# Optimization experiments

Hardware: AMD Instinct MI355X
Metric: run time of the kernel (lower is better)

The kernel has to match this reference:

```python
import jax, jax.numpy as jnp
import numpy as np

H = 224          # image height (self.shape[0])
W_IMG = 224      # image width (self.shape[1])
CELLS = 7        # mask_generator num_cells
PAD = CELLS // 2 # reflect pad size
D = 512          # encoder feature dim
NUM_BATCHES = 30
BATCH = 100
EPS = 1e-8       # torch CosineSimilarity eps


def _encode(xb, Wenc):
    # stand-in encoder: 32x32 block average pool -> [B,3,7,7] -> linear to D
    B = xb.shape[0]
    feats = xb.reshape(B, 3, CELLS, H // CELLS, CELLS, W_IMG // CELLS).mean(axis=(3, 5))
    return feats.reshape(B, -1) @ Wenc  # [B, D]


def _cosine(a, b):
    # a: [1,D] (h_star), b: [B,D]; matches nn.CosineSimilarity(dim=1)
    num = jnp.sum(a * b, axis=1)
    den = jnp.maximum(jnp.linalg.norm(a, axis=1) * jnp.linalg.norm(b, axis=1), EPS)
    return num / den  # [B]


def _make_masks(grid, sx, sy):
    # grid: [B,1,7,7] binary floats; bilinear upsample, reflect pad, shifted crop
    B = grid.shape[0]
    up = jax.image.resize(grid, (B, 1, H, W_IMG), method='linear')
    padded = jnp.pad(up, ((0, 0), (0, 0), (PAD, PAD), (PAD, PAD)), mode='reflect')
    crop = jax.vmap(
        lambda g, i, j: jax.lax.dynamic_slice(g, (0, i, j), (1, H, W_IMG))
    )(padded, sx, sy)
    return crop  # [B,1,H,W]


def _relax(x, Wenc, grids, shifts_x, shifts_y):
    h_star = _encode(x, Wenc)  # [1, D]
    R0 = jnp.zeros((H, W_IMG), jnp.float32)
    U0 = jnp.zeros_like(R0)
    sow0 = jnp.full((H, W_IMG), 1e-10, jnp.float32)

    def sample_step(carry, inp):
        # sequential weighted running-mean / Welford variance update
        R, U, sow = carry
        s, m = inp  # s: scalar sim, m: [H,W] mask
        sow = sow + m
        R_new = R + m * (s - R) / sow
        U = U + (s - R_new) * (s - R) * m
        return (R_new, U, sow), None

    def batch_step(carry, binp):
        grid, sx, sy = binp
        masks = _make_masks(grid, sx, sy)        # [B,1,H,W]
        x_mask = x * masks                       # fill_vals_zeros=True path
        h = _encode(x_mask, Wenc)                # [B,D]
        sims = _cosine(h_star, h)                # [B]
        carry, _ = jax.lax.scan(sample_step, carry, (sims, masks[:, 0]))
        return carry, None

    (R, U, sow), _ = jax.lax.scan(batch_step, (R0, U0, sow0),
                                  (grids, shifts_x, shifts_y))
    uncertainty = U / (sow - 1.0)
    return jnp.stack([R, uncertainty])  # [2,H,W]: importance, uncertainty


def setup_inputs() -> dict:
    key = jax.random.key(0)
    k1, k2, k3, k4, k5 = jax.random.split(key, 5)
    x = jax.random.normal(k1, (1, 3, H, W_IMG), jnp.float32)
    Wenc = jax.random.normal(k2, (3 * CELLS * CELLS, D), jnp.float32) * 0.05
    grids = (jax.random.uniform(k3, (NUM_BATCHES, BATCH, 1, CELLS, CELLS)) < 0.5).astype(jnp.float32)
    shifts_x = jax.random.randint(k4, (NUM_BATCHES, BATCH), 0, CELLS)
    shifts_y = jax.random.randint(k5, (NUM_BATCHES, BATCH), 0, CELLS)
    return {"x": x, "Wenc": Wenc, "grids": grids,
            "shifts_x": shifts_x, "shifts_y": shifts_y}


def reference(x, Wenc, grids, shifts_x, shifts_y):
    return _relax(x, Wenc, grids, shifts_x, shifts_y)
```

## Files before the change

kernel.cpp:

```cpp
#include <hip/hip_runtime.h>
#include <math.h>

#define NS 3000
#define NF 147
#define ND 512
#define NSIG 49
#define NSAMP 4
#define NHBLK 750

#define OFF_WT     0
#define OFF_FEATS  6272
#define OFF_V      6432
#define OFF_T      236928
#define OFF_G      589952

__device__ __forceinline__ void wt_compute(int sigma, int p, int& i0c, int& i1c,
                                           float& w0, float& w1) {
  int k = p + sigma - 3;
  int r = k < 0 ? -k : (k > 223 ? 446 - k : k);
  float tc = (float)(2 * r - 31) * (1.0f / 64.0f);
  float fl = floorf(tc);
  int i0 = (int)fl;
  float fr = tc - fl;
  i0c = min(max(i0, 0), 6);
  i1c = min(max(i0 + 1, 0), 6);
  w0 = 1.0f - fr;
  w1 = fr;
}

__global__ void __launch_bounds__(256) k_initV(const float* __restrict__ x,
                                               float* __restrict__ ws) {
  int b = blockIdx.x;
  int t = threadIdx.x;
  if (b < NF) {
    int c = b / 49, rem = b % 49, cy = rem / 7, cx = rem % 7;
    float acc = 0.f;
    for (int idx = t; idx < 1024; idx += 256) {
      int yy = idx >> 5, xx = idx & 31;
      acc += x[(c * 224 + cy * 32 + yy) * 224 + cx * 32 + xx];
    }
    for (int off = 32; off; off >>= 1) acc += __shfl_down(acc, off);
    __shared__ float red[4];
    int wave = t >> 6, lane = t & 63;
    if (lane == 0) red[wave] = acc;
    __syncthreads();
    if (t == 0) ws[OFF_FEATS + b] = (red[0] + red[1] + red[2] + red[3]) * (1.0f / 1024.0f);
  } else if (b == NF) {
    float4* WT = (float4*)(ws + OFF_WT);
    for (int e = t; e < 7 * 224; e += 256) {
      int sigma = e / 224, p = e % 224;
      int i0c, i1c; float w0, w1;
      wt_compute(sigma, p, i0c, i1c, w0, w1);
      WT[e] = make_float4(w0, w1, __int_as_float(i0c), __int_as_float(i1c));
    }
  } else {
    int tid = (b - NF - 1) * 256 + t;
    if (tid >= 7 * 3 * 224 * 7) return;
    int cx = tid % 7;
    int y  = (tid / 7) % 224;
    int c  = (tid / (7 * 224)) % 3;
    int sy = tid / (7 * 224 * 3);
    float acc[7];
    #pragma unroll
    for (int g = 0; g < 7; ++g) acc[g] = 0.f;
    const float* xrow = x + (c * 224 + y) * 224;
    for (int x0 = 0; x0 < 32; ++x0) {
      int px = cx * 32 + x0;
      int i0, i1; float w0, w1;
      wt_compute(sy, px, i0, i1, w0, w1);
      float v = xrow[px];
      #pragma unroll
      for (int g = 0; g < 7; ++g) {
        float w = (g == i0 ? w0 : 0.f) + (g == i1 ? w1 : 0.f);
        acc[g] = fmaf(w, v, acc[g]);
      }
    }
    float* Vp = ws + OFF_V + (((sy * 3 + c) * 224 + y) * 49 + cx * 7);
    #pragma unroll
    for (int g = 0; g < 7; ++g) Vp[g] = acc[g];
  }
}

__global__ void __launch_bounds__(256) k_T(float* __restrict__ ws) {
  int tid = blockIdx.x * blockDim.x + threadIdx.x;
  if (tid >= NSIG * NF * 49) {
    int e = tid - NSIG * NF * 49;
    if (e < 7203) ws[OFF_G + e] = 0.f;
    return;
  }
  int g = tid % 49;
  int f = (tid / 49) % NF;
  int sig = tid / (49 * NF);
  int sx = sig / 7, sy = sig % 7;
  int gy = g / 7, gx = g % 7;
  int c = f / 49, rem = f % 49, cy = rem / 7, cx = rem % 7;
  const float4* WT = (const float4*)(ws + OFF_WT);
  const float* V = ws + OFF_V + ((sy * 3 + c) * 224) * 49 + cx * 7 + gx;
  float acc = 0.f;
  for (int y0 = 0; y0 < 32; ++y0) {
    int y = cy * 32 + y0;
    float4 wt = WT[sx * 224 + y];
    int i0 = __float_as_int(wt.z), i1 = __float_as_int(wt.w);
    float w = (gy == i0 ? wt.x : 0.f) + (gy == i1 ? wt.y : 0.f);
    acc = fmaf(w, V[y * 49], acc);
  }
  ws[OFF_T + (sig * 49 + g) * NF + f] = acc * (1.0f / 1024.0f);
}

__global__ void __launch_bounds__(256) k_H2s(const float* __restrict__ Wenc,
                                             const float* __restrict__ grids,
                                             const int* __restrict__ shx,
                                             const int* __restrict__ shy,
                                             float* __restrict__ ws) {
  __shared__ __align__(16) float sF[NF * NSAMP];
  __shared__ float sGr[NSAMP * 49];
  __shared__ float sFeat[NF];
  __shared__ int   sSig[NSAMP];
  __shared__ float sRed[2][NSAMP][4];
  __shared__ float sRedH[4];
  __shared__ float sS[NSAMP];
  int t = threadIdx.x;
  int b = blockIdx.x;
  int i0s = b * NSAMP;
  for (int e = t; e < NSAMP * 49; e += 256) sGr[e] = grids[i0s * 49 + e];
  if (t < NSAMP) sSig[t] = shx[i0s + t] * 7 + shy[i0s + t];
  if (t < NF) sFeat[t] = ws[OFF_FEATS + t];
  __syncthreads();
  for (int idx = t; idx < NF * NSAMP; idx += 256) {
    int r = idx / NF, f = idx - r * NF;
    const float* T2 = ws + OFF_T + sSig[r] * (49 * NF) + f;
    const float* gr = sGr + r * 49;
    float acc = 0.f;
    #pragma unroll
    for (int g = 0; g < 49; ++g) acc = fmaf(T2[g * NF], gr[g], acc);
    sF[f * NSAMP + r] = acc;
  }
  __syncthreads();
  float accA[NSAMP], accB[NSAMP];
  #pragma unroll
  for (int r = 0; r < NSAMP; ++r) { accA[r] = 0.f; accB[r] = 0.f; }
  float h0 = 0.f, h1 = 0.f;
  const float* W0 = Wenc + t;
  const float* W1 = Wenc + t + 256;
  const float4* sF4 = (const float4*)sF;
  for (int f = 0; f < NF; ++f) {
    float w0 = W0[f * ND];
    float w1 = W1[f * ND];
    float fe = sFeat[f];
    h0 = fmaf(fe, w0, h0);
    h1 = fmaf(fe, w1, h1);
    float4 a4 = sF4[f];
    float a[NSAMP] = {a4.x, a4.y, a4.z, a4.w};
    #pragma unroll
    for (int r = 0; r < NSAMP; ++r) {
      accA[r] = fmaf(a[r], w0, accA[r]);
      accB[r] = fmaf(a[r], w1, accB[r]);
    }
  }
  int wave = t >> 6, lane = t & 63;
  float hq = h0 * h0 + h1 * h1;
  for (int off = 32; off; off >>= 1) hq += __shfl_down(hq, off);
  if (lane == 0) sRedH[wave] = hq;
  #pragma unroll
  for (int r = 0; r < NSAMP; ++r) {
    float np = accA[r] * h0 + accB[r] * h1;
    float sp = accA[r] * accA[r] + accB[r] * accB[r];
    for (int off = 32; off; off >>= 1) {
      np += __shfl_down(np, off);
      sp += __shfl_down(sp, off);
    }
    if (lane == 0) { sRed[0][r][wave] = np; sRed[1][r][wave] = sp; }
  }
  __syncthreads();
  if (t == 0) sRedH[0] = sqrtf(sRedH[0] + sRedH[1] + sRedH[2] + sRedH[3]);
  __syncthreads();
  if (t < NSAMP) {
    float np = sRed[0][t][0] + sRed[0][t][1] + sRed[0][t][2] + sRed[0][t][3];
    float sp = sRed[1][t][0] + sRed[1][t][1] + sRed[1][t][2] + sRed[1][t][3];
    float den = fmaxf(sRedH[0] * sqrtf(sp), 1e-8f);
    sS[t] = np / den;
  }
  __syncthreads();
  for (int e = t; e < NSAMP * 3 * 49; e += 256) {
    int k = e % 49;
    int rp = e / 49;
    int r = rp / 3, p = rp - r * 3;
    float gv = sGr[r * 49 + k];
    if (gv != 0.f) {
      float s = sS[r];
      float add = (p == 0) ? 1.f : ((p == 1) ? s : s * s);
      atomicAdd(&ws[OFF_G + p * 2401 + sSig[r] * 49 + k], add);
    }
  }
}

__global__ void __launch_bounds__(256) k_CO(const float* __restrict__ ws,
                                            float* __restrict__ out) {
  __shared__ float Gl[3 * 2401];
  __shared__ float sC[NF];
  int b = blockIdx.x;
  int t = threadIdx.x;
  for (int e = t; e < 3 * 2401; e += 256) Gl[e] = ws[OFF_G + e];
  __syncthreads();
  const float4* WT = (const float4*)(ws + OFF_WT);
  if (t < NF) {
    int k = t / 49, r = t - k * 49;
    int sx = r / 7, gy = r % 7;
    float acc = 0.f;
    for (int sy = 0; sy < 7; ++sy) {
      float4 wt = WT[sy * 224 + b];
      int i0 = __float_as_int(wt.z), i1 = __float_as_int(wt.w);
      int base = k * 2401 + (sx * 7 + sy) * 49 + gy * 7;
      acc += wt.x * Gl[base + i0] + wt.y * Gl[base + i1];
    }
    sC[t] = acc;
  }
  __syncthreads();
  if (t < 224) {
    int py = t;
    float S0 = 0.f, S1 = 0.f, S2 = 0.f;
    for (int sx = 0; sx < 7; ++sx) {
      float4 wt = WT[sx * 224 + py];
      int i0 = __float_as_int(wt.z), i1 = __float_as_int(wt.w);
      int base = sx * 7;
      S0 += wt.x * sC[base + i0]      + wt.y * sC[base + i1];
      S1 += wt.x * sC[49 + base + i0] + wt.y * sC[49 + base + i1];
      S2 += wt.x * sC[98 + base + i0] + wt.y * sC[98 + base + i1];
    }
    float W = 1e-10f + S0;
    float R = S1 / W;
    float U = S2 - S1 * S1 / W;
    out[py * 224 + b] = R;
    out[224 * 224 + py * 224 + b] = U / (W - 1.0f);
  }
}

extern "C" void kernel_launch(void* const* d_in, const int* in_sizes, int n_in,
                              void* d_out, int out_size, void* d_ws, size_t ws_size,
                              hipStream_t stream) {
  const float* x     = (const float*)d_in[0];
  const float* Wenc  = (const float*)d_in[1];
  const float* grids = (const float*)d_in[2];
  const int*   shx   = (const int*)d_in[3];
  const int*   shy   = (const int*)d_in[4];
  float* out = (float*)d_out;
  float* ws  = (float*)d_ws;

  int vblocks = (7 * 3 * 224 * 7 + 255) / 256;
  k_initV<<<NF + 1 + vblocks, 256, 0, stream>>>(x, ws);
  k_T<<<(NSIG * NF * 49 + 7203 + 255) / 256, 256, 0, stream>>>(ws);
  k_H2s<<<NHBLK, 256, 0, stream>>>(Wenc, grids, shx, shy, ws);
  k_CO<<<224, 256, 0, stream>>>(ws, out);
}
```

Baseline: 108.8 us.

## Fuse V and T precompute into one tiled kernel using shared memory

Merges the separate V-projection and T-projection kernels into a single kernel in which each block loads one 32x32 image cell into shared memory. The block runs the horizontal and vertical bilinear-weight contractions from LDS, with no global V intermediate and one fewer launch. The encoder matmul in k_H2s also switches to float2 loads of Wenc. That reassigns each thread to adjacent output columns, so the h0/h1 accumulation order differs but the reductions stay equivalent. The fused kernel recomputes weights per block and loads each cell's x tile once for each of the 7 sy values.

```diff
diff --git a/kernel.cpp b/kernel.cpp
--- a/kernel.cpp
+++ b/kernel.cpp
@@ -7,10 +7,10 @@
 #define NSIG 49
 #define NSAMP 4
 #define NHBLK 750
+#define NBLK_VT 1029
 
 #define OFF_WT     0
 #define OFF_FEATS  6272
-#define OFF_V      6432
 #define OFF_T      236928
 #define OFF_G      589952
 
@@ -28,83 +28,93 @@
   w1 = fr;
 }
 
-__global__ void __launch_bounds__(256) k_initV(const float* __restrict__ x,
-                                               float* __restrict__ ws) {
+__global__ void __launch_bounds__(256) k_VT(const float* __restrict__ x,
+                                            float* __restrict__ ws) {
   int b = blockIdx.x;
   int t = threadIdx.x;
-  if (b < NF) {
-    int c = b / 49, rem = b % 49, cy = rem / 7, cx = rem % 7;
-    float acc = 0.f;
-    for (int idx = t; idx < 1024; idx += 256) {
-      int yy = idx >> 5, xx = idx & 31;
-      acc += x[(c * 224 + cy * 32 + yy) * 224 + cx * 32 + xx];
-    }
+  if (b >= NBLK_VT) {
+    if (b == NBLK_VT) {
+      float4* WT = (float4*)(ws + OFF_WT);
+      for (int e = t; e < 7 * 224; e += 256) {
+        int sigma = e / 224, p = e % 224;
+        int i0c, i1c; float w0, w1;
+        wt_compute(sigma, p, i0c, i1c, w0, w1);
+        WT[e] = make_float4(w0, w1, __int_as_float(i0c), __int_as_float(i1c));
+      }
+    } else {
+      int e = (b - NBLK_VT - 1) * 256 + t;
+      if (e < 3 * 2401) ws[OFF_G + e] = 0.f;
+    }
+    return;
+  }
+
+  __shared__ float sX[32][33];
+  __shared__ float sV[32][8];
+  __shared__ float4 sWX[32];
+  __shared__ float4 sWY[7][32];
+  __shared__ float red[4];
+
+  int f = b % NF;
+  int sy = b / NF;
+  int c = f / 49, rem = f % 49, cy = rem / 7, cx = rem % 7;
+
+  const float* xb = x + (c * 224 + cy * 32) * 224 + cx * 32;
+  float psum = 0.f;
+  for (int idx = t; idx < 1024; idx += 256) {
+    int yy = idx >> 5, xx = idx & 31;
+    float v = xb[yy * 224 + xx];
+    sX[yy][xx] = v;
+    psum += v;
+  }
+
+  if (t < 32) {
+    int i0, i1; float w0, w1;
+    wt_compute(sy, cx * 32 + t, i0, i1, w0, w1);
+    sWX[t] = make_float4(w0, w1, __int_as_float(i0), __int_as_float(i1));
+  } else if (t < 32 + 224) {
+    int e = t - 32;
+    int sx = e >> 5, y0 = e & 31;
+    int i0, i1; float w0, w1;
+    wt_compute(sx, cy * 32 + y0, i0, i1, w0, w1);
+    sWY[sx][y0] = make_float4(w0, w1, __int_as_float(i0), __int_as_float(i1));
+  }
+
+  if (sy == 0) {
+    float acc = psum;
     for (int off = 32; off; off >>= 1) acc += __shfl_down(acc, off);
-    __shared__ float red[4];
     int wave = t >> 6, lane = t & 63;
     if (lane == 0) red[wave] = acc;
-    __syncthreads();
-    if (t == 0) ws[OFF_FEATS + b] = (red[0] + red[1] + red[2] + red[3]) * (1.0f / 1024.0f);
-  } else if (b == NF) {
-    float4* WT = (float4*)(ws + OFF_WT);
-    for (int e = t; e < 7 * 224; e += 256) {
-      int sigma = e / 224, p = e % 224;
-      int i0c, i1c; float w0, w1;
-      wt_compute(sigma, p, i0c, i1c, w0, w1);
-      WT[e] = make_float4(w0, w1, __int_as_float(i0c), __int_as_float(i1c));
-    }
-  } else {
-    int tid = (b - NF - 1) * 256 + t;
-    if (tid >= 7 * 3 * 224 * 7) return;
-    int cx = tid % 7;
-    int y  = (tid / 7) % 224;
-    int c  = (tid / (7 * 224)) % 3;
-    int sy = tid / (7 * 224 * 3);
-    float acc[7];
-    #pragma unroll
-    for (int g = 0; g < 7; ++g) acc[g] = 0.f;
-    const float* xrow = x + (c * 224 + y) * 224;
+  }
+  __syncthreads();
+  if (sy == 0 && t == 0)
+    ws[OFF_FEATS + f] = (red[0] + red[1] + red[2] + red[3]) * (1.0f / 1024.0f);
+
+  if (t < 224) {
+    int y0 = t / 7, gx = t % 7;
+    float acc = 0.f;
+    #pragma unroll
     for (int x0 = 0; x0 < 32; ++x0) {
-      int px = cx * 32 + x0;
-      int i0, i1; float w0, w1;
-      wt_compute(sy, px, i0, i1, w0, w1);
-      float v = xrow[px];
-      #pragma unroll
-      for (int g = 0; g < 7; ++g) {
-        float w = (g == i0 ? w0 : 0.f) + (g == i1 ? w1 : 0.f);
-        acc[g] = fmaf(w, v, acc[g]);
-      }
-    }
-    float* Vp = ws + OFF_V + (((sy * 3 + c) * 224 + y) * 49 + cx * 7);
-    #pragma unroll
-    for (int g = 0; g < 7; ++g) Vp[g] = acc[g];
-  }
-}
-
-__global__ void __launch_bounds__(256) k_T(float* __restrict__ ws) {
-  int tid = blockIdx.x * blockDim.x + threadIdx.x;
-  if (tid >= NSIG * NF * 49) {
-    int e = tid - NSIG * NF * 49;
-    if (e < 7203) ws[OFF_G + e] = 0.f;
-    return;
-  }
-  int g = tid % 49;
-  int f = (tid / 49) % NF;
-  int sig = tid / (49 * NF);
-  int sx = sig / 7, sy = sig % 7;
-  int gy = g / 7, gx = g % 7;
-  int c = f / 49, rem = f % 49, cy = rem / 7, cx = rem % 7;
-  const float4* WT = (const float4*)(ws + OFF_WT);
-  const float* V = ws + OFF_V + ((sy * 3 + c) * 224) * 49 + cx * 7 + gx;
-  float acc = 0.f;
-  for (int y0 = 0; y0 < 32; ++y0) {
-    int y = cy * 32 + y0;
-    float4 wt = WT[sx * 224 + y];
-    int i0 = __float_as_int(wt.z), i1 = __float_as_int(wt.w);
-    float w = (gy == i0 ? wt.x : 0.f) + (gy == i1 ? wt.y : 0.f);
-    acc = fmaf(w, V[y * 49], acc);
-  }
-  ws[OFF_T + (sig * 49 + g) * NF + f] = acc * (1.0f / 1024.0f);
+      float4 wt = sWX[x0];
+      int i0 = __float_as_int(wt.z), i1 = __float_as_int(wt.w);
+      float w = (gx == i0 ? wt.x : 0.f) + (gx == i1 ? wt.y : 0.f);
+      acc = fmaf(w, sX[y0][x0], acc);
+    }
+    sV[y0][gx] = acc;
+  }
+  __syncthreads();
+
+  for (int e = t; e < 343; e += 256) {
+    int sx = e / 49, r2 = e % 49, gy = r2 / 7, gx = r2 % 7;
+    float acc = 0.f;
+    #pragma unroll
+    for (int y0 = 0; y0 < 32; ++y0) {
+      float4 wt = sWY[sx][y0];
+      int i0 = __float_as_int(wt.z), i1 = __float_as_int(wt.w);
+      float w = (gy == i0 ? wt.x : 0.f) + (gy == i1 ? wt.y : 0.f);
+      acc = fmaf(w, sV[y0][gx], acc);
+    }
+    ws[OFF_T + ((sx * 7 + sy) * 49 + gy * 7 + gx) * NF + f] = acc * (1.0f / 1024.0f);
+  }
 }
 
 __global__ void __launch_bounds__(256) k_H2s(const float* __restrict__ Wenc,
@@ -140,21 +150,19 @@
   #pragma unroll
   for (int r = 0; r < NSAMP; ++r) { accA[r] = 0.f; accB[r] = 0.f; }
   float h0 = 0.f, h1 = 0.f;
-  const float* W0 = Wenc + t;
-  const float* W1 = Wenc + t + 256;
+  const float2* W2 = (const float2*)Wenc;
   const float4* sF4 = (const float4*)sF;
   for (int f = 0; f < NF; ++f) {
-    float w0 = W0[f * ND];
-    float w1 = W1[f * ND];
+    float2 w = W2[f * (ND / 2) + t];
     float fe = sFeat[f];
-    h0 = fmaf(fe, w0, h0);
-    h1 = fmaf(fe, w1, h1);
+    h0 = fmaf(fe, w.x, h0);
+    h1 = fmaf(fe, w.y, h1);
     float4 a4 = sF4[f];
     float a[NSAMP] = {a4.x, a4.y, a4.z, a4.w};
     #pragma unroll
     for (int r = 0; r < NSAMP; ++r) {
-      accA[r] = fmaf(a[r], w0, accA[r]);
-      accB[r] = fmaf(a[r], w1, accB[r]);
+      accA[r] = fmaf(a[r], w.x, accA[r]);
+      accB[r] = fmaf(a[r], w.y, accB[r]);
     }
   }
   int wave = t >> 6, lane = t & 63;
@@ -246,9 +254,7 @@
   float* out = (float*)d_out;
   float* ws  = (float*)d_ws;
 
-  int vblocks = (7 * 3 * 224 * 7 + 255) / 256;
-  k_initV<<<NF + 1 + vblocks, 256, 0, stream>>>(x, ws);
-  k_T<<<(NSIG * NF * 49 + 7203 + 255) / 256, 256, 0, stream>>>(ws);
+  k_VT<<<NBLK_VT + 1 + 29, 256, 0, stream>>>(x, ws);
   k_H2s<<<NHBLK, 256, 0, stream>>>(Wenc, grids, shx, shy, ws);
   k_CO<<<224, 256, 0, stream>>>(ws, out);
 }
```

After: 101.5 us. 1.07x faster.
